# Kernel tuning notes

Measured on AMD Instinct MI355X. Metric: run time of the kernel, lower is better.

## Reference

```python
import jax, jax.numpy as jnp
import numpy as np

# ---- Cl(4,1) geometric-product Cayley table (32 blades, metric diag(+,+,+,+,-)) ----
def _build_gp_map():
    metric = [1.0, 1.0, 1.0, 1.0, -1.0]  # e1..e4 square to +1, e5 squares to -1
    gp = np.zeros((32, 32, 32), dtype=np.float32)
    for a in range(32):          # blade a as a bitmask over 5 generators
        for b in range(32):
            # sign from reordering generators into canonical order
            swaps = 0
            t = a >> 1
            while t:
                swaps += bin(t & b).count('1')
                t >>= 1
            sign = -1.0 if (swaps & 1) else 1.0
            # sign from contracted (repeated) generators via the metric
            common = a & b
            for i in range(5):
                if common & (1 << i):
                    sign *= metric[i]
            gp[a, b, a ^ b] = sign  # e_a * e_b = sign * e_{a xor b}
    return gp

GP_MAP = _build_gp_map()  # [32, 32, 32], highly sparse (one nonzero per (a,b))
EPS = 1e-6

B, S, IN, OUT = 2, 1024, 256, 256

def setup_inputs() -> dict:
    key = jax.random.key(0)
    k1, k2 = jax.random.split(key)
    x = jax.random.normal(k1, (B, S, IN, 32), dtype=jnp.float32)
    std = 1.0 / float(np.sqrt(IN * 32))  # grade-aware Xavier scale from reset_parameters
    weight = jax.random.normal(k2, (OUT, IN, 32), dtype=jnp.float32) * std
    return {"x": x, "weight": weight}

def normalize_cl41(mv):
    # normalize each multivector by its coefficient magnitude over the 32 lanes
    norm = jnp.sqrt(jnp.sum(mv * mv, axis=-1, keepdims=True) + EPS)
    return mv / norm

def reference(x, weight):
    gp = jnp.asarray(GP_MAP, dtype=x.dtype)
    # W_op[o,i,l,k] = sum_j weight[o,i,j] * gp[j,l,k]
    W_op = jnp.einsum('oij,jlk->oilk', weight, gp)
    # out[b,s,o,k] = sum_{i,l} x[b,s,i,l] * W_op[o,i,l,k]
    out = jnp.einsum('bsil,oilk->bsok', x, W_op)
    return normalize_cl41(out)
```

## Files before the change

kernel.cpp:

```cpp
#include <hip/hip_runtime.h>
#include <hip/hip_bf16.h>
#include <stdint.h>

typedef _Float16 f16;
typedef __attribute__((ext_vector_type(8))) _Float16 f16x8;
typedef __attribute__((ext_vector_type(4))) float f32x4;

#define M_DIM 2048
#define K_FULL 8192
#define M2 8192
#define K2 2048
#define N2 2048
#define BM 128
#define BN 128
#define BK 32
#define PSTR 132

struct CMat { int re[4][4]; int im[4][4]; };

constexpr CMat cmul(const CMat& A, const CMat& B) {
  CMat C{};
  for (int r = 0; r < 4; ++r)
    for (int c = 0; c < 4; ++c) {
      int re = 0, im = 0;
      for (int t = 0; t < 4; ++t) {
        re += A.re[r][t] * B.re[t][c] - A.im[r][t] * B.im[t][c];
        im += A.re[r][t] * B.im[t][c] + A.im[r][t] * B.re[t][c];
      }
      C.re[r][c] = re; C.im[r][c] = im;
    }
  return C;
}

constexpr int gp_sign_ct(int a, int b) {
  int sw = 0;
  for (int t = a >> 1; t; t >>= 1) {
    int x = t & b;
    while (x) { sw += x & 1; x >>= 1; }
  }
  int s = (sw & 1) ? -1 : 1;
  if ((a & b) & 16) s = -s;
  return s;
}

struct Tables {
  int8_t f_idx[32][4]; int8_t f_sgn[32][4];
  int8_t g_idx[32][4]; int8_t g_sgn[32][4];
  bool ok;
};

constexpr Tables make_tables() {
  CMat G[5] = {
    { {{0,0,0,1},{0,0,1,0},{0,1,0,0},{1,0,0,0}},
      {{0,0,0,0},{0,0,0,0},{0,0,0,0},{0,0,0,0}} },
    { {{0,0,0,0},{0,0,0,0},{0,0,0,0},{0,0,0,0}},
      {{0,0,0,-1},{0,0,1,0},{0,-1,0,0},{1,0,0,0}} },
    { {{0,0,1,0},{0,0,0,-1},{1,0,0,0},{0,-1,0,0}},
      {{0,0,0,0},{0,0,0,0},{0,0,0,0},{0,0,0,0}} },
    { {{0,0,0,0},{0,0,0,0},{0,0,0,0},{0,0,0,0}},
      {{0,0,-1,0},{0,0,0,-1},{1,0,0,0},{0,1,0,0}} },
    { {{0,0,0,0},{0,0,0,0},{0,0,0,0},{0,0,0,0}},
      {{1,0,0,0},{0,1,0,0},{0,0,-1,0},{0,0,0,-1}} } };
  CMat ID{ {{1,0,0,0},{0,1,0,0},{0,0,1,0},{0,0,0,1}},
           {{0,0,0,0},{0,0,0,0},{0,0,0,0},{0,0,0,0}} };
  CMat U[32] = {};
  for (int A = 0; A < 32; ++A) {
    CMat u = ID;
    for (int b = 0; b < 5; ++b) if (A & (1 << b)) u = cmul(u, G[b]);
    U[A] = u;
  }
  bool ok = true;
  for (int a = 0; a < 32; ++a)
    for (int b = 0; b < 32; ++b) {
      CMat P = cmul(U[a], U[b]);
      int s = gp_sign_ct(a, b);
      const CMat& T = U[a ^ b];
      for (int r = 0; r < 4; ++r)
        for (int c = 0; c < 4; ++c)
          if (P.re[r][c] != s * T.re[r][c] || P.im[r][c] != s * T.im[r][c]) ok = false;
    }
  Tables t{};
  int cnt[32] = {};
  for (int A = 0; A < 32; ++A) {
    int n = 0;
    for (int r = 0; r < 4; ++r)
      for (int c = 0; c < 4; ++c) {
        int vr = U[A].re[r][c], vi = U[A].im[r][c];
        if (vr) {
          int s = (r * 4 + c) * 2;
          if (n < 4 && cnt[s] < 4) {
            t.g_idx[A][n] = (int8_t)s; t.g_sgn[A][n] = (int8_t)vr;
            t.f_idx[s][cnt[s]] = (int8_t)A; t.f_sgn[s][cnt[s]] = (int8_t)vr;
            cnt[s]++;
          } else ok = false;
          n++;
        }
        if (vi) {
          int s = (r * 4 + c) * 2 + 1;
          if (n < 4 && cnt[s] < 4) {
            t.g_idx[A][n] = (int8_t)s; t.g_sgn[A][n] = (int8_t)vi;
            t.f_idx[s][cnt[s]] = (int8_t)A; t.f_sgn[s][cnt[s]] = (int8_t)vi;
            cnt[s]++;
          } else ok = false;
          n++;
        }
      }
    if (n != 4) ok = false;
  }
  for (int s = 0; s < 32; ++s) if (cnt[s] != 4) ok = false;
  t.ok = ok;
  return t;
}

constexpr Tables HT = make_tables();
static_assert(HT.ok, "Cl(4,1) -> M(4,C) homomorphism check FAILED");


__device__ __forceinline__ void async16(const f16* g, f16* l) {
  __builtin_amdgcn_global_load_lds(
      (const __attribute__((address_space(1))) uint32_t*)g,
      (__attribute__((address_space(3))) uint32_t*)l,
      16, 0, 0);
}

__device__ __forceinline__ float gp_sign_rt(int a, int b) {
  int sw = 0;
  for (int t = a >> 1; t; t >>= 1) sw += __popc(t & b);
  float s = (sw & 1) ? -1.0f : 1.0f;
  if ((a & b) & 16) s = -s;
  return s;
}

__global__ __launch_bounds__(256) void fwd_x_kernel(const float* __restrict__ x,
                                                    f16* __restrict__ Ag) {
  int tid = blockIdx.x * 256 + threadIdx.x;
  int m = tid >> 8, i = tid & 255;
  const float4* xp = (const float4*)(x + (size_t)tid * 32);
  float xv[32];
#pragma unroll
  for (int q = 0; q < 8; ++q) {
    float4 v = xp[q];
    xv[q * 4] = v.x; xv[q * 4 + 1] = v.y; xv[q * 4 + 2] = v.z; xv[q * 4 + 3] = v.w;
  }
  float sv[32];
#pragma unroll
  for (int s = 0; s < 32; ++s)
    sv[s] = (float)HT.f_sgn[s][0] * xv[HT.f_idx[s][0]]
          + (float)HT.f_sgn[s][1] * xv[HT.f_idx[s][1]]
          + (float)HT.f_sgn[s][2] * xv[HT.f_idx[s][2]]
          + (float)HT.f_sgn[s][3] * xv[HT.f_idx[s][3]];
#pragma unroll
  for (int c = 0; c < 4; ++c) {
    f16x8 h;
#pragma unroll
    for (int e = 0; e < 8; ++e) {
      int t = e >> 1, p = e & 1;
      h[e] = (f16)sv[t * 8 + c * 2 + p];
    }
    *(f16x8*)(Ag + ((size_t)(m * 4 + c)) * K2 + i * 8) = h;
  }
}

__global__ __launch_bounds__(256) void fwd_w_kernel(const float* __restrict__ w,
                                                    f16* __restrict__ Bt) {
  int tid = blockIdx.x * 256 + threadIdx.x;
  int o = tid >> 8, i = tid & 255;
  const float4* wp = (const float4*)(w + (size_t)tid * 32);
  float wv[32];
#pragma unroll
  for (int q = 0; q < 8; ++q) {
    float4 v = wp[q];
    wv[q * 4] = v.x; wv[q * 4 + 1] = v.y; wv[q * 4 + 2] = v.z; wv[q * 4 + 3] = v.w;
  }
  float sv[32];
#pragma unroll
  for (int s = 0; s < 32; ++s)
    sv[s] = (float)HT.f_sgn[s][0] * wv[HT.f_idx[s][0]]
          + (float)HT.f_sgn[s][1] * wv[HT.f_idx[s][1]]
          + (float)HT.f_sgn[s][2] * wv[HT.f_idx[s][2]]
          + (float)HT.f_sgn[s][3] * wv[HT.f_idx[s][3]];
#pragma unroll
  for (int r = 0; r < 4; ++r)
#pragma unroll
    for (int q = 0; q < 2; ++q) {
      f16x8 h;
#pragma unroll
      for (int e = 0; e < 8; ++e) {
        int t = e >> 1, p = e & 1;
        float re = sv[(r * 4 + t) * 2], im = sv[(r * 4 + t) * 2 + 1];
        float v = (q == 0) ? (p == 0 ? re : -im) : (p == 0 ? im : re);
        h[e] = (f16)v;
      }
      *(f16x8*)(Bt + ((size_t)(o * 8 + r * 2 + q)) * K2 + i * 8) = h;
    }
}

__global__ __launch_bounds__(256) void gemm_fused_kernel(const f16* __restrict__ A,
                                                         const f16* __restrict__ Bw,
                                                         float* __restrict__ out) {
  __shared__ __align__(16) char smem[BM * PSTR * 4];
  f16* As = (f16*)smem;
  f16* Bs = (f16*)(smem + BM * BK * 2);
  float* ps = (float*)smem;
  const int t = threadIdx.x;
  const int wave = t >> 6, lane = t & 63;
  const int wr = wave >> 1, wc = wave & 1;
  const int g = lane >> 4, lc = lane & 15;
  const int m0 = blockIdx.y * BM, n0 = blockIdx.x * BN;

  f32x4 acc[4][4];
#pragma unroll
  for (int i = 0; i < 4; ++i)
#pragma unroll
    for (int j = 0; j < 4; ++j) {
      acc[i][j][0] = 0.f; acc[i][j][1] = 0.f; acc[i][j][2] = 0.f; acc[i][j][3] = 0.f;
    }

  const f16* agp[2]; const f16* bgp[2];
  f16* alp[2]; f16* blp[2];
#pragma unroll
  for (int q = 0; q < 2; ++q) {
    int chunk = (q << 8) + (wave << 6) + lane;
    int row = chunk >> 2;
    int gk = ((chunk & 3) ^ ((row >> 1) & 3)) << 3;
    agp[q] = A  + (size_t)(m0 + row) * K2 + gk;
    bgp[q] = Bw + (size_t)(n0 + row) * K2 + gk;
    alp[q] = As + (q << 11) + (wave << 9);
    blp[q] = Bs + (q << 11) + (wave << 9);
  }

  const int swz = (lc >> 1) & 3;
  int aoff[4], boff[4];
#pragma unroll
  for (int i = 0; i < 4; ++i) {
    aoff[i] = ((wr << 6) + (i << 4) + lc) * BK + ((g ^ swz) << 3);
    boff[i] = ((wc << 6) + (i << 4) + lc) * BK + ((g ^ swz) << 3);
  }

  for (int kk = 0; kk < K2; kk += BK) {
    async16(agp[0] + kk, alp[0]);
    async16(agp[1] + kk, alp[1]);
    async16(bgp[0] + kk, blp[0]);
    async16(bgp[1] + kk, blp[1]);
    __syncthreads();

    f16x8 av[4], bv[4];
#pragma unroll
    for (int i = 0; i < 4; ++i) av[i] = *(const f16x8*)(As + aoff[i]);
#pragma unroll
    for (int i = 0; i < 4; ++i) bv[i] = *(const f16x8*)(Bs + boff[i]);
#pragma unroll
    for (int tm = 0; tm < 4; ++tm)
#pragma unroll
      for (int tn = 0; tn < 4; ++tn)
        acc[tm][tn] = __builtin_amdgcn_mfma_f32_16x16x32_f16(av[tm], bv[tn],
                                                             acc[tm][tn], 0, 0, 0);
    __syncthreads();
  }

#pragma unroll
  for (int tm = 0; tm < 4; ++tm) {
    int rowb = (wr << 6) + (tm << 4) + (g << 2);
#pragma unroll
    for (int tn = 0; tn < 4; ++tn) {
      int col = (wc << 6) + (tn << 4) + lc;
#pragma unroll
      for (int r = 0; r < 4; ++r)
        ps[(rowb + r) * PSTR + col] = acc[tm][tn][r];
    }
  }
  __syncthreads();

#pragma unroll
  for (int pi = 0; pi < 2; ++pi) {
    int p = (pi << 8) + t;
    int mh = p >> 4, oh = p & 15;
    float yv[4][8];
#pragma unroll
    for (int c = 0; c < 4; ++c) {
      const float* row = ps + (mh * 4 + c) * PSTR + oh * 8;
      *(float4*)&yv[c][0] = *(const float4*)row;
      *(float4*)&yv[c][4] = *(const float4*)(row + 4);
    }
    float ss = 0.f;
#pragma unroll
    for (int c = 0; c < 4; ++c)
#pragma unroll
      for (int j = 0; j < 8; ++j) ss += yv[c][j] * yv[c][j];
    float inv = rsqrtf(0.25f * ss + 1e-6f);

    float ov[32];
#pragma unroll
    for (int k = 0; k < 32; ++k) {
      float v = 0.f;
#pragma unroll
      for (int j = 0; j < 4; ++j) {
        constexpr const int8_t (*GI)[4] = HT.g_idx;
        int s = HT.g_idx[k][j];
        int cell = s >> 1;
        int rr = cell >> 2, cc = cell & 3, pp = s & 1;
        float sgn = (float)HT.g_sgn[k][j];
        v += sgn * yv[cc][rr * 2 + pp];
        (void)GI;
      }
      ov[k] = v * 0.25f * inv;
    }
    int m = (m0 >> 2) + mh;
    int o = (n0 >> 3) + oh;
    float* op = out + (size_t)m * 8192 + o * 32;
#pragma unroll
    for (int q = 0; q < 8; ++q)
      *(float4*)(op + q * 4) = make_float4(ov[q * 4], ov[q * 4 + 1],
                                           ov[q * 4 + 2], ov[q * 4 + 3]);
  }
}

__global__ __launch_bounds__(256) void naive_vl_kernel(const float* __restrict__ x,
                                                       const float* __restrict__ w,
                                                       float* __restrict__ out) {
  __shared__ float xs[8192];
  __shared__ float sgt[1024];
  int m = blockIdx.x, o0 = blockIdx.y << 3;
  int t = threadIdx.x;
  for (int i = t; i < 1024; i += 256) {
    int kk = i >> 5, ll = i & 31;
    sgt[i] = gp_sign_rt(kk ^ ll, ll);
  }
  const float4* xr = (const float4*)(x + (size_t)m * K_FULL);
  float4* xs4 = (float4*)xs;
  for (int i = t; i < 2048; i += 256) xs4[i] = xr[i];
  __syncthreads();
  int k = t & 31, ol = t >> 5;
  int o = o0 + ol;
  const float* wrow = w + (size_t)o * K_FULL;
  float acc = 0.f;
  for (int l = 0; l < 32; ++l) {
    float s = sgt[(k << 5) + l];
    const float* wp = wrow + (k ^ l);
    const float* xp = xs + l;
    float part = 0.f;
#pragma unroll 8
    for (int i = 0; i < 256; ++i) part += xp[i << 5] * wp[i << 5];
    acc += part * s;
  }
  float ss = acc * acc;
  for (int msk = 1; msk < 32; msk <<= 1) ss += __shfl_xor(ss, msk, 32);
  out[((size_t)m * 256 + o) * 32 + k] = acc * rsqrtf(ss + 1e-6f);
}

extern "C" void kernel_launch(void* const* d_in, const int* in_sizes, int n_in,
                              void* d_out, int out_size, void* d_ws, size_t ws_size,
                              hipStream_t stream) {
  const float* x = (const float*)d_in[0];
  const float* w = (const float*)d_in[1];
  float* out = (float*)d_out;

  size_t agE = (size_t)M2 * K2;
  size_t btE = (size_t)N2 * K2;
  size_t need = (agE + btE) * sizeof(f16);

  if (ws_size >= need) {
    f16* Ag = (f16*)d_ws;
    f16* Bt = Ag + agE;
    fwd_x_kernel<<<dim3(M_DIM), dim3(256), 0, stream>>>(x, Ag);
    fwd_w_kernel<<<dim3(256), dim3(256), 0, stream>>>(w, Bt);
    gemm_fused_kernel<<<dim3(N2 / BN, M2 / BM), dim3(256), 0, stream>>>(Ag, Bt, out);
  } else {
    naive_vl_kernel<<<dim3(M_DIM, 32), dim3(256), 0, stream>>>(x, w, out);
  }
}
```

Before: 232.2 us.

## Stage preprocessing loads through LDS and halve GEMM epilogue shared memory

```diff
diff --git a/kernel.cpp b/kernel.cpp
--- a/kernel.cpp
+++ b/kernel.cpp
@@ -133,15 +133,17 @@
 
 __global__ __launch_bounds__(256) void fwd_x_kernel(const float* __restrict__ x,
                                                     f16* __restrict__ Ag) {
-  int tid = blockIdx.x * 256 + threadIdx.x;
-  int m = tid >> 8, i = tid & 255;
-  const float4* xp = (const float4*)(x + (size_t)tid * 32);
-  float xv[32];
-#pragma unroll
-  for (int q = 0; q < 8; ++q) {
-    float4 v = xp[q];
-    xv[q * 4] = v.x; xv[q * 4 + 1] = v.y; xv[q * 4 + 2] = v.z; xv[q * 4 + 3] = v.w;
-  }
+  __shared__ float xs[256 * 33];
+  const int m = blockIdx.x, t = threadIdx.x;
+  const float4* src = (const float4*)(x + (size_t)m * 8192);
+#pragma unroll
+  for (int c = t; c < 2048; c += 256) {
+    float4 v = src[c];
+    float* d = xs + (c >> 3) * 33 + ((c & 7) << 2);
+    d[0] = v.x; d[1] = v.y; d[2] = v.z; d[3] = v.w;
+  }
+  __syncthreads();
+  const float* xv = xs + t * 33;
   float sv[32];
 #pragma unroll
   for (int s = 0; s < 32; ++s)
@@ -154,24 +156,26 @@
     f16x8 h;
 #pragma unroll
     for (int e = 0; e < 8; ++e) {
-      int t = e >> 1, p = e & 1;
-      h[e] = (f16)sv[t * 8 + c * 2 + p];
-    }
-    *(f16x8*)(Ag + ((size_t)(m * 4 + c)) * K2 + i * 8) = h;
+      int tt = e >> 1, p = e & 1;
+      h[e] = (f16)sv[tt * 8 + c * 2 + p];
+    }
+    *(f16x8*)(Ag + ((size_t)(m * 4 + c)) * K2 + t * 8) = h;
   }
 }
 
 __global__ __launch_bounds__(256) void fwd_w_kernel(const float* __restrict__ w,
                                                     f16* __restrict__ Bt) {
-  int tid = blockIdx.x * 256 + threadIdx.x;
-  int o = tid >> 8, i = tid & 255;
-  const float4* wp = (const float4*)(w + (size_t)tid * 32);
-  float wv[32];
-#pragma unroll
-  for (int q = 0; q < 8; ++q) {
-    float4 v = wp[q];
-    wv[q * 4] = v.x; wv[q * 4 + 1] = v.y; wv[q * 4 + 2] = v.z; wv[q * 4 + 3] = v.w;
-  }
+  __shared__ float xs[256 * 33];
+  const int o = blockIdx.x, t = threadIdx.x;
+  const float4* src = (const float4*)(w + (size_t)o * 8192);
+#pragma unroll
+  for (int c = t; c < 2048; c += 256) {
+    float4 v = src[c];
+    float* d = xs + (c >> 3) * 33 + ((c & 7) << 2);
+    d[0] = v.x; d[1] = v.y; d[2] = v.z; d[3] = v.w;
+  }
+  __syncthreads();
+  const float* wv = xs + t * 33;
   float sv[32];
 #pragma unroll
   for (int s = 0; s < 32; ++s)
@@ -186,19 +190,19 @@
       f16x8 h;
 #pragma unroll
       for (int e = 0; e < 8; ++e) {
-        int t = e >> 1, p = e & 1;
-        float re = sv[(r * 4 + t) * 2], im = sv[(r * 4 + t) * 2 + 1];
+        int tt = e >> 1, p = e & 1;
+        float re = sv[(r * 4 + tt) * 2], im = sv[(r * 4 + tt) * 2 + 1];
         float v = (q == 0) ? (p == 0 ? re : -im) : (p == 0 ? im : re);
         h[e] = (f16)v;
       }
-      *(f16x8*)(Bt + ((size_t)(o * 8 + r * 2 + q)) * K2 + i * 8) = h;
+      *(f16x8*)(Bt + ((size_t)(o * 8 + r * 2 + q)) * K2 + t * 8) = h;
     }
 }
 
 __global__ __launch_bounds__(256) void gemm_fused_kernel(const f16* __restrict__ A,
                                                          const f16* __restrict__ Bw,
                                                          float* __restrict__ out) {
-  __shared__ __align__(16) char smem[BM * PSTR * 4];
+  __shared__ __align__(16) char smem[64 * PSTR * 4];
   f16* As = (f16*)smem;
   f16* Bs = (f16*)(smem + BM * BK * 2);
   float* ps = (float*)smem;
@@ -259,22 +263,24 @@
   }
 
 #pragma unroll
-  for (int tm = 0; tm < 4; ++tm) {
-    int rowb = (wr << 6) + (tm << 4) + (g << 2);
-#pragma unroll
-    for (int tn = 0; tn < 4; ++tn) {
-      int col = (wc << 6) + (tn << 4) + lc;
-#pragma unroll
-      for (int r = 0; r < 4; ++r)
-        ps[(rowb + r) * PSTR + col] = acc[tm][tn][r];
-    }
-  }
-  __syncthreads();
-
-#pragma unroll
-  for (int pi = 0; pi < 2; ++pi) {
-    int p = (pi << 8) + t;
-    int mh = p >> 4, oh = p & 15;
+  for (int half = 0; half < 2; ++half) {
+    if (half) __syncthreads();
+    if (wr == half) {
+#pragma unroll
+      for (int tm = 0; tm < 4; ++tm) {
+        int rowl = (tm << 4) + (g << 2);
+#pragma unroll
+        for (int tn = 0; tn < 4; ++tn) {
+          int col = (wc << 6) + (tn << 4) + lc;
+#pragma unroll
+          for (int r = 0; r < 4; ++r)
+            ps[(rowl + r) * PSTR + col] = acc[tm][tn][r];
+        }
+      }
+    }
+    __syncthreads();
+
+    const int mh = t >> 4, oh = t & 15;
     float yv[4][8];
 #pragma unroll
     for (int c = 0; c < 4; ++c) {
@@ -295,17 +301,15 @@
       float v = 0.f;
 #pragma unroll
       for (int j = 0; j < 4; ++j) {
-        constexpr const int8_t (*GI)[4] = HT.g_idx;
         int s = HT.g_idx[k][j];
         int cell = s >> 1;
         int rr = cell >> 2, cc = cell & 3, pp = s & 1;
         float sgn = (float)HT.g_sgn[k][j];
         v += sgn * yv[cc][rr * 2 + pp];
-        (void)GI;
       }
       ov[k] = v * 0.25f * inv;
     }
-    int m = (m0 >> 2) + mh;
+    int m = (m0 >> 2) + (half << 4) + mh;
     int o = (n0 >> 3) + oh;
     float* op = out + (size_t)m * 8192 + o * 32;
 #pragma unroll
```

Result: no change. 232.1 us (-0.1%).
